# Performance work log

Hardware: AMD Instinct MI355X
Metric: run time of the kernel (lower is better)

## Reference

```python
import jax, jax.numpy as jnp
import numpy as np

EMBED = 768
HEADS = 12
D_K = EMBED // HEADS  # 64


def setup_inputs() -> dict:
    key = jax.random.key(0)
    ks = jax.random.split(key, 9)
    w_scale = EMBED ** -0.5
    inp = {
        "x": jax.random.normal(ks[0], (128, 256, 1, EMBED), dtype=jnp.float32),
        "Wq": jax.random.normal(ks[1], (EMBED, EMBED), dtype=jnp.float32) * w_scale,
        "bq": jax.random.normal(ks[2], (EMBED,), dtype=jnp.float32) * 0.02,
        "Wk": jax.random.normal(ks[3], (EMBED, EMBED), dtype=jnp.float32) * w_scale,
        "bk": jax.random.normal(ks[4], (EMBED,), dtype=jnp.float32) * 0.02,
        "Wv": jax.random.normal(ks[5], (EMBED, EMBED), dtype=jnp.float32) * w_scale,
        "bv": jax.random.normal(ks[6], (EMBED,), dtype=jnp.float32) * 0.02,
        "Wo": jax.random.normal(ks[7], (EMBED, EMBED), dtype=jnp.float32) * w_scale,
        "bo": jax.random.normal(ks[8], (EMBED,), dtype=jnp.float32) * 0.02,
    }
    return inp


def reference(x, Wq, bq, Wk, bk, Wv, bv, Wo, bo):
    # x: (n_rows r, n_cols i/j, batch n, embed)
    R, C, B, E = x.shape
    H, Dk = HEADS, D_K
    # tied-row scaling: d_k^{-1/2} / sqrt(n_rows)
    scaling = (Dk ** -0.5) / np.sqrt(R).astype(np.float32)

    q = (x @ Wq.T + bq).reshape(R, C, B, H, Dk) * scaling
    k = (x @ Wk.T + bk).reshape(R, C, B, H, Dk)
    v = (x @ Wv.T + bv).reshape(R, C, B, H, Dk)

    # scores summed over rows r and head dim d -> (h, n, i, j)
    scores = jnp.einsum('rinhd,rjnhd->hnij', q, k)
    probs = jax.nn.softmax(scores, axis=-1)  # dropout p=0 -> identity

    # shared attention applied per row
    c = jnp.einsum('hnij,rjnhd->rinhd', probs, v).reshape(R, C, B, E)
    out = c @ Wo.T + bo
    return (out, probs)
```

## Files before the change

kernel.cpp:

```cpp
#include <hip/hip_runtime.h>
#include <math.h>

typedef short bf16x8 __attribute__((ext_vector_type(8)));
typedef float f32x4 __attribute__((ext_vector_type(4)));
typedef unsigned short ushort8 __attribute__((ext_vector_type(8)));

constexpr int R = 128, Cc = 256, E = 768, H = 12;
constexpr int M = R * Cc;
constexpr size_t TOK = (size_t)M * E;

__device__ __forceinline__ unsigned short f2b(float f) {
  unsigned int u = __float_as_uint(f);
  u += 0x7fff + ((u >> 16) & 1);
  return (unsigned short)(u >> 16);
}

__device__ __forceinline__ void ldst16(const unsigned short* g, unsigned short* l) {
  __builtin_amdgcn_global_load_lds(
      (const __attribute__((address_space(1))) unsigned int*)g,
      (__attribute__((address_space(3))) unsigned int*)l, 16, 0, 0);
}

__global__ __launch_bounds__(256) void cvt_bf16(const float* __restrict__ in,
                                                unsigned short* __restrict__ out,
                                                int n8) {
  int i = blockIdx.x * 256 + threadIdx.x;
  if (i >= n8) return;
  const float4* p = (const float4*)in;
  float4 a = p[2 * i], b = p[2 * i + 1];
  ushort8 o;
  o[0] = f2b(a.x); o[1] = f2b(a.y); o[2] = f2b(a.z); o[3] = f2b(a.w);
  o[4] = f2b(b.x); o[5] = f2b(b.y); o[6] = f2b(b.z); o[7] = f2b(b.w);
  ((ushort8*)out)[i] = o;
}

template <int MODE>
__global__ __launch_bounds__(256) void proj_mfma(
    const unsigned short* __restrict__ A, const unsigned short* __restrict__ B,
    const float* __restrict__ bias, void* __restrict__ Yv, float scale) {
  constexpr int K = 768, N = 768;
  __shared__ unsigned short As[128 * 32];
  __shared__ unsigned short Bs[128 * 32];
  const int tid = threadIdx.x, wv = tid >> 6, ln = tid & 63;
  const int n0 = blockIdx.x * 128, m0 = blockIdx.y * 128;
  const int wm = (wv & 1) * 64, wn = (wv >> 1) * 64;
  const int srow = ln >> 2, scol = (ln & 3) * 8;
  f32x4 acc[4][4] = {};
  for (int k0 = 0; k0 < K; k0 += 32) {
    __syncthreads();
#pragma unroll
    for (int t = 0; t < 2; ++t) {
      const int ch = wv * 2 + t;
      const int row = ch * 16 + srow;
      ldst16(A + (size_t)(m0 + row) * K + k0 + scol, As + ch * 512 + ln * 8);
      ldst16(B + (size_t)(n0 + row) * K + k0 + scol, Bs + ch * 512 + ln * 8);
    }
    __syncthreads();
    bf16x8 a[4], b[4];
#pragma unroll
    for (int i = 0; i < 4; ++i)
      a[i] = *(const bf16x8*)(As + (wm + i * 16 + (ln & 15)) * 32 + (ln >> 4) * 8);
#pragma unroll
    for (int j = 0; j < 4; ++j)
      b[j] = *(const bf16x8*)(Bs + (wn + j * 16 + (ln & 15)) * 32 + (ln >> 4) * 8);
#pragma unroll
    for (int i = 0; i < 4; ++i)
#pragma unroll
      for (int j = 0; j < 4; ++j)
        acc[i][j] = __builtin_amdgcn_mfma_f32_16x16x32_bf16(a[i], b[j], acc[i][j], 0, 0, 0);
  }
#pragma unroll
  for (int j = 0; j < 4; ++j) {
    const int n = n0 + wn + j * 16 + (ln & 15);
    const float bn = bias[n];
#pragma unroll
    for (int i = 0; i < 4; ++i) {
#pragma unroll
      for (int r = 0; r < 4; ++r) {
        const int m = m0 + wm + i * 16 + (ln >> 4) * 4 + r;
        const float v = (acc[i][j][r] + bn) * scale;
        if (MODE == 0)      ((unsigned short*)Yv)[(size_t)m * N + n] = f2b(v);
        else if (MODE == 1) ((unsigned short*)Yv)[(size_t)n * M + m] = f2b(v);
        else                ((float*)Yv)[(size_t)m * N + n] = v;
      }
    }
  }
}

__global__ __launch_bounds__(256) void qk_mfma(const unsigned short* __restrict__ q,
                                               const unsigned short* __restrict__ k,
                                               float* __restrict__ Sp) {
  __shared__ unsigned short As[64 * 64];
  __shared__ unsigned short Bs[64 * 64];
  const int tid = threadIdx.x, wv = tid >> 6, ln = tid & 63;
  const int i0 = (blockIdx.x & 3) * 64, j0 = (blockIdx.x >> 2) * 64;
  const int h = blockIdx.y, kc = blockIdx.z;
  const int wm = (wv & 1) * 32, wn = (wv >> 1) * 32;
  const int srow = ln >> 3, scol = (ln & 7) * 8;
  f32x4 acc[2][2] = {};
  for (int rr = 0; rr < 32; ++rr) {
    const int r = kc * 32 + rr;
    __syncthreads();
#pragma unroll
    for (int t = 0; t < 2; ++t) {
      const int ch = wv * 2 + t;
      const int row = ch * 8 + srow;
      ldst16(q + (size_t)(r * Cc + i0 + row) * E + h * 64 + scol, As + ch * 512 + ln * 8);
      ldst16(k + (size_t)(r * Cc + j0 + row) * E + h * 64 + scol, Bs + ch * 512 + ln * 8);
    }
    __syncthreads();
#pragma unroll
    for (int dk = 0; dk < 2; ++dk) {
      bf16x8 a[2], b[2];
#pragma unroll
      for (int i = 0; i < 2; ++i)
        a[i] = *(const bf16x8*)(As + (wm + i * 16 + (ln & 15)) * 64 + dk * 32 + (ln >> 4) * 8);
#pragma unroll
      for (int j = 0; j < 2; ++j)
        b[j] = *(const bf16x8*)(Bs + (wn + j * 16 + (ln & 15)) * 64 + dk * 32 + (ln >> 4) * 8);
#pragma unroll
      for (int i = 0; i < 2; ++i)
#pragma unroll
        for (int j = 0; j < 2; ++j)
          acc[i][j] = __builtin_amdgcn_mfma_f32_16x16x32_bf16(a[i], b[j], acc[i][j], 0, 0, 0);
    }
  }
  const size_t base = ((size_t)kc * H + h) * Cc * Cc;
#pragma unroll
  for (int i = 0; i < 2; ++i)
#pragma unroll
    for (int j = 0; j < 2; ++j)
#pragma unroll
      for (int r4 = 0; r4 < 4; ++r4) {
        const int ii = i0 + wm + i * 16 + (ln >> 4) * 4 + r4;
        const int jj = j0 + wn + j * 16 + (ln & 15);
        Sp[base + (size_t)ii * Cc + jj] = acc[i][j][r4];
      }
}

__global__ __launch_bounds__(256) void softmax_k(const float* __restrict__ Sp,
                                                 float* __restrict__ P,
                                                 unsigned short* __restrict__ Pb) {
  const int row = blockIdx.x, j = threadIdx.x;
  const size_t stride = (size_t)H * Cc * Cc;
  const size_t base = (size_t)row * Cc + j;
  float s = Sp[base] + Sp[base + stride] + Sp[base + 2 * stride] + Sp[base + 3 * stride];
  float m = s;
#pragma unroll
  for (int o = 32; o > 0; o >>= 1) m = fmaxf(m, __shfl_xor(m, o));
  __shared__ float sm[4], ss[4];
  const int wid = j >> 6, lane = j & 63;
  if (lane == 0) sm[wid] = m;
  __syncthreads();
  m = fmaxf(fmaxf(sm[0], sm[1]), fmaxf(sm[2], sm[3]));
  float e = expf(s - m);
  float t = e;
#pragma unroll
  for (int o = 32; o > 0; o >>= 1) t += __shfl_xor(t, o);
  if (lane == 0) ss[wid] = t;
  __syncthreads();
  t = ss[0] + ss[1] + ss[2] + ss[3];
  const float p = e / t;
  P[base] = p;
  Pb[base] = f2b(p);
}

__global__ __launch_bounds__(256) void pv_mfma(const unsigned short* __restrict__ P,
                                               const unsigned short* __restrict__ V,
                                               unsigned short* __restrict__ Co) {
  __shared__ unsigned short As[64 * 64];
  __shared__ unsigned short Bs[64 * 64];
  const int tid = threadIdx.x, wv = tid >> 6, ln = tid & 63;
  const int i0 = blockIdx.x * 64;
  const int r = blockIdx.y, h = blockIdx.z;
  const int wm = (wv & 1) * 32, wn = (wv >> 1) * 32;
  const int srow = ln >> 3, scol = (ln & 7) * 8;
  f32x4 acc[2][2] = {};
  for (int jc = 0; jc < 4; ++jc) {
    const int j0 = jc * 64;
    __syncthreads();
#pragma unroll
    for (int t = 0; t < 2; ++t) {
      const int ch = wv * 2 + t;
      const int row = ch * 8 + srow;
      ldst16(P + ((size_t)h * Cc + i0 + row) * Cc + j0 + scol, As + ch * 512 + ln * 8);
      ldst16(V + (size_t)(h * 64 + row) * M + r * Cc + j0 + scol, Bs + ch * 512 + ln * 8);
    }
    __syncthreads();
#pragma unroll
    for (int dk = 0; dk < 2; ++dk) {
      bf16x8 a[2], b[2];
#pragma unroll
      for (int i = 0; i < 2; ++i)
        a[i] = *(const bf16x8*)(As + (wm + i * 16 + (ln & 15)) * 64 + dk * 32 + (ln >> 4) * 8);
#pragma unroll
      for (int j = 0; j < 2; ++j)
        b[j] = *(const bf16x8*)(Bs + (wn + j * 16 + (ln & 15)) * 64 + dk * 32 + (ln >> 4) * 8);
#pragma unroll
      for (int i = 0; i < 2; ++i)
#pragma unroll
        for (int j = 0; j < 2; ++j)
          acc[i][j] = __builtin_amdgcn_mfma_f32_16x16x32_bf16(a[i], b[j], acc[i][j], 0, 0, 0);
    }
  }
#pragma unroll
  for (int i = 0; i < 2; ++i)
#pragma unroll
    for (int j = 0; j < 2; ++j)
#pragma unroll
      for (int r4 = 0; r4 < 4; ++r4) {
        const int mm = i0 + wm + i * 16 + (ln >> 4) * 4 + r4;
        const int nn = wn + j * 16 + (ln & 15);
        Co[((size_t)r * Cc + mm) * E + h * 64 + nn] = f2b(acc[i][j][r4]);
      }
}

extern "C" void kernel_launch(void* const* d_in, const int* in_sizes, int n_in,
                              void* d_out, int out_size, void* d_ws, size_t ws_size,
                              hipStream_t stream) {
  const float* x  = (const float*)d_in[0];
  const float* Wq = (const float*)d_in[1];
  const float* bq = (const float*)d_in[2];
  const float* Wk = (const float*)d_in[3];
  const float* bk = (const float*)d_in[4];
  const float* Wv = (const float*)d_in[5];
  const float* bv = (const float*)d_in[6];
  const float* Wo = (const float*)d_in[7];
  const float* bo = (const float*)d_in[8];
  float* out = (float*)d_out;
  float* probs = out + TOK;

  char* ws = (char*)d_ws;
  unsigned short* x_bf  = (unsigned short*)(ws);
  unsigned short* q_bf  = (unsigned short*)(ws + 50331648);
  unsigned short* k_bf  = (unsigned short*)(ws + 100663296);
  unsigned short* vT_bf = (unsigned short*)(ws + 150994944);
  unsigned short* Wq_bf = (unsigned short*)(ws + 201326592);
  unsigned short* Wk_bf = Wq_bf + 589824;
  unsigned short* Wv_bf = Wk_bf + 589824;
  unsigned short* Wo_bf = Wv_bf + 589824;
  float* S_part         = (float*)(ws + 206045184);
  unsigned short* P_bf  = (unsigned short*)(ws + 218628096);
  unsigned short* c_bf  = q_bf;

  const float scaling = 0.125f / sqrtf(128.f);

  cvt_bf16<<<12288, 256, 0, stream>>>(x, x_bf, 3145728);
  cvt_bf16<<<288, 256, 0, stream>>>(Wq, Wq_bf, 73728);
  cvt_bf16<<<288, 256, 0, stream>>>(Wk, Wk_bf, 73728);
  cvt_bf16<<<288, 256, 0, stream>>>(Wv, Wv_bf, 73728);
  cvt_bf16<<<288, 256, 0, stream>>>(Wo, Wo_bf, 73728);

  dim3 gp(6, 256);
  proj_mfma<0><<<gp, 256, 0, stream>>>(x_bf, Wq_bf, bq, q_bf, scaling);
  proj_mfma<0><<<gp, 256, 0, stream>>>(x_bf, Wk_bf, bk, k_bf, 1.0f);
  proj_mfma<1><<<gp, 256, 0, stream>>>(x_bf, Wv_bf, bv, vT_bf, 1.0f);

  qk_mfma<<<dim3(16, H, 4), 256, 0, stream>>>(q_bf, k_bf, S_part);
  softmax_k<<<H * Cc, 256, 0, stream>>>(S_part, probs, P_bf);
  pv_mfma<<<dim3(4, R, H), 256, 0, stream>>>(P_bf, vT_bf, c_bf);

  proj_mfma<2><<<gp, 256, 0, stream>>>(c_bf, Wo_bf, bo, out, 1.0f);
}
```

Baseline: 539.8 us.

## Fuse QKV projection and relayout Q/K/V for large-tile attention GEMMs

Merges the three Q/K/V projections into one launch over a concatenated weight matrix. Its epilogue writes Q and K in a head-major layout where the row index and head dim form one contiguous reduction axis, and writes V transposed per head. That lets the QK and PV stages run as plain 128x128-tile GEMMs with 64-wide K steps through a shared gemm_core, replacing the small 64x64 tiles that reloaded one row at a time. QK split-K goes from 4 to 8 partials, so softmax sums eight partial score buffers. The cost is scattered 2-byte stores in the projection epilogue and more partial-score traffic.

```diff
diff --git a/kernel.cpp b/kernel.cpp
--- a/kernel.cpp
+++ b/kernel.cpp
@@ -34,107 +34,104 @@
   ((ushort8*)out)[i] = o;
 }
 
-template <int MODE>
-__global__ __launch_bounds__(256) void proj_mfma(
-    const unsigned short* __restrict__ A, const unsigned short* __restrict__ B,
-    const float* __restrict__ bias, void* __restrict__ Yv, float scale) {
-  constexpr int K = 768, N = 768;
-  __shared__ unsigned short As[128 * 32];
-  __shared__ unsigned short Bs[128 * 32];
-  const int tid = threadIdx.x, wv = tid >> 6, ln = tid & 63;
-  const int n0 = blockIdx.x * 128, m0 = blockIdx.y * 128;
-  const int wm = (wv & 1) * 64, wn = (wv >> 1) * 64;
-  const int srow = ln >> 2, scol = (ln & 3) * 8;
-  f32x4 acc[4][4] = {};
-  for (int k0 = 0; k0 < K; k0 += 32) {
+template <int KITERS>
+__device__ __forceinline__ void gemm_core(
+    const unsigned short* __restrict__ Aptr, size_t Astride,
+    const unsigned short* __restrict__ Bptr, size_t Bstride,
+    unsigned short* As, unsigned short* Bs, int wv, int ln, f32x4 acc[4][4]) {
+  const int srow = ln >> 3, scol = (ln & 7) * 8;
+  const int wm = (wv & 1) * 64, wn = (wv >> 1) * 64;
+#pragma unroll 1
+  for (int kt = 0; kt < KITERS; ++kt) {
+    const int k0 = kt * 64;
     __syncthreads();
 #pragma unroll
-    for (int t = 0; t < 2; ++t) {
-      const int ch = wv * 2 + t;
-      const int row = ch * 16 + srow;
-      ldst16(A + (size_t)(m0 + row) * K + k0 + scol, As + ch * 512 + ln * 8);
-      ldst16(B + (size_t)(n0 + row) * K + k0 + scol, Bs + ch * 512 + ln * 8);
+    for (int t = 0; t < 4; ++t) {
+      const int ch = wv * 4 + t;
+      const int row = ch * 8 + srow;
+      ldst16(Aptr + (size_t)row * Astride + k0 + scol, As + ch * 512 + ln * 8);
+      ldst16(Bptr + (size_t)row * Bstride + k0 + scol, Bs + ch * 512 + ln * 8);
     }
     __syncthreads();
-    bf16x8 a[4], b[4];
-#pragma unroll
-    for (int i = 0; i < 4; ++i)
-      a[i] = *(const bf16x8*)(As + (wm + i * 16 + (ln & 15)) * 32 + (ln >> 4) * 8);
-#pragma unroll
-    for (int j = 0; j < 4; ++j)
-      b[j] = *(const bf16x8*)(Bs + (wn + j * 16 + (ln & 15)) * 32 + (ln >> 4) * 8);
-#pragma unroll
-    for (int i = 0; i < 4; ++i)
+#pragma unroll
+    for (int dk = 0; dk < 2; ++dk) {
+      bf16x8 a[4], b[4];
+#pragma unroll
+      for (int i = 0; i < 4; ++i)
+        a[i] = *(const bf16x8*)(As + (wm + i * 16 + (ln & 15)) * 64 + dk * 32 + (ln >> 4) * 8);
 #pragma unroll
       for (int j = 0; j < 4; ++j)
-        acc[i][j] = __builtin_amdgcn_mfma_f32_16x16x32_bf16(a[i], b[j], acc[i][j], 0, 0, 0);
-  }
+        b[j] = *(const bf16x8*)(Bs + (wn + j * 16 + (ln & 15)) * 64 + dk * 32 + (ln >> 4) * 8);
+#pragma unroll
+      for (int i = 0; i < 4; ++i)
+#pragma unroll
+        for (int j = 0; j < 4; ++j)
+          acc[i][j] = __builtin_amdgcn_mfma_f32_16x16x32_bf16(a[i], b[j], acc[i][j], 0, 0, 0);
+    }
+  }
+}
+
+__global__ __launch_bounds__(256) void qkv_mfma(
+    const unsigned short* __restrict__ A, const unsigned short* __restrict__ B,
+    const float* __restrict__ bq, const float* __restrict__ bk,
+    const float* __restrict__ bv, unsigned short* __restrict__ qp,
+    unsigned short* __restrict__ kp, unsigned short* __restrict__ vp, float scale) {
+  __shared__ unsigned short As[128 * 64];
+  __shared__ unsigned short Bs[128 * 64];
+  const int tid = threadIdx.x, wv = tid >> 6, ln = tid & 63;
+  const int n0 = blockIdx.x * 128, m0 = blockIdx.y * 128;
+  const int wm = (wv & 1) * 64, wn = (wv >> 1) * 64;
+  f32x4 acc[4][4] = {};
+  gemm_core<12>(A + (size_t)m0 * E, E, B + (size_t)n0 * E, E, As, Bs, wv, ln, acc);
+  const int part = n0 / 768;
+  const float* bias = part == 0 ? bq : (part == 1 ? bk : bv);
+  const float sc = part == 0 ? scale : 1.0f;
 #pragma unroll
   for (int j = 0; j < 4; ++j) {
     const int n = n0 + wn + j * 16 + (ln & 15);
-    const float bn = bias[n];
-#pragma unroll
-    for (int i = 0; i < 4; ++i) {
-#pragma unroll
-      for (int r = 0; r < 4; ++r) {
-        const int m = m0 + wm + i * 16 + (ln >> 4) * 4 + r;
-        const float v = (acc[i][j][r] + bn) * scale;
-        if (MODE == 0)      ((unsigned short*)Yv)[(size_t)m * N + n] = f2b(v);
-        else if (MODE == 1) ((unsigned short*)Yv)[(size_t)n * M + m] = f2b(v);
-        else                ((float*)Yv)[(size_t)m * N + n] = v;
-      }
-    }
-  }
-}
-
-__global__ __launch_bounds__(256) void qk_mfma(const unsigned short* __restrict__ q,
-                                               const unsigned short* __restrict__ k,
+    const int nn = n - part * 768;
+    const int h = nn >> 6, d = nn & 63;
+    const float bn = bias[nn];
+#pragma unroll
+    for (int i = 0; i < 4; ++i)
+#pragma unroll
+      for (int r4 = 0; r4 < 4; ++r4) {
+        const int m = m0 + wm + i * 16 + (ln >> 4) * 4 + r4;
+        const int r = m >> 8, ii = m & 255;
+        const unsigned short val = f2b((acc[i][j][r4] + bn) * sc);
+        if (part == 0)
+          qp[((size_t)(h * 256 + ii) << 13) + r * 64 + d] = val;
+        else if (part == 1)
+          kp[((size_t)(h * 256 + ii) << 13) + r * 64 + d] = val;
+        else
+          vp[((size_t)(h * 8192 + r * 64 + d) << 8) + ii] = val;
+      }
+  }
+}
+
+__global__ __launch_bounds__(256) void qk_mfma(const unsigned short* __restrict__ qp,
+                                               const unsigned short* __restrict__ kp,
                                                float* __restrict__ Sp) {
-  __shared__ unsigned short As[64 * 64];
-  __shared__ unsigned short Bs[64 * 64];
-  const int tid = threadIdx.x, wv = tid >> 6, ln = tid & 63;
-  const int i0 = (blockIdx.x & 3) * 64, j0 = (blockIdx.x >> 2) * 64;
+  __shared__ unsigned short As[128 * 64];
+  __shared__ unsigned short Bs[128 * 64];
+  const int tid = threadIdx.x, wv = tid >> 6, ln = tid & 63;
+  const int m0 = (blockIdx.x & 1) * 128, n0 = (blockIdx.x >> 1) * 128;
   const int h = blockIdx.y, kc = blockIdx.z;
-  const int wm = (wv & 1) * 32, wn = (wv >> 1) * 32;
-  const int srow = ln >> 3, scol = (ln & 7) * 8;
-  f32x4 acc[2][2] = {};
-  for (int rr = 0; rr < 32; ++rr) {
-    const int r = kc * 32 + rr;
-    __syncthreads();
-#pragma unroll
-    for (int t = 0; t < 2; ++t) {
-      const int ch = wv * 2 + t;
-      const int row = ch * 8 + srow;
-      ldst16(q + (size_t)(r * Cc + i0 + row) * E + h * 64 + scol, As + ch * 512 + ln * 8);
-      ldst16(k + (size_t)(r * Cc + j0 + row) * E + h * 64 + scol, Bs + ch * 512 + ln * 8);
-    }
-    __syncthreads();
-#pragma unroll
-    for (int dk = 0; dk < 2; ++dk) {
-      bf16x8 a[2], b[2];
-#pragma unroll
-      for (int i = 0; i < 2; ++i)
-        a[i] = *(const bf16x8*)(As + (wm + i * 16 + (ln & 15)) * 64 + dk * 32 + (ln >> 4) * 8);
-#pragma unroll
-      for (int j = 0; j < 2; ++j)
-        b[j] = *(const bf16x8*)(Bs + (wn + j * 16 + (ln & 15)) * 64 + dk * 32 + (ln >> 4) * 8);
-#pragma unroll
-      for (int i = 0; i < 2; ++i)
-#pragma unroll
-        for (int j = 0; j < 2; ++j)
-          acc[i][j] = __builtin_amdgcn_mfma_f32_16x16x32_bf16(a[i], b[j], acc[i][j], 0, 0, 0);
-    }
-  }
-  const size_t base = ((size_t)kc * H + h) * Cc * Cc;
-#pragma unroll
-  for (int i = 0; i < 2; ++i)
-#pragma unroll
-    for (int j = 0; j < 2; ++j)
-#pragma unroll
-      for (int r4 = 0; r4 < 4; ++r4) {
-        const int ii = i0 + wm + i * 16 + (ln >> 4) * 4 + r4;
-        const int jj = j0 + wn + j * 16 + (ln & 15);
-        Sp[base + (size_t)ii * Cc + jj] = acc[i][j][r4];
+  const int wm = (wv & 1) * 64, wn = (wv >> 1) * 64;
+  f32x4 acc[4][4] = {};
+  const size_t hb = (size_t)h * 256 * 8192 + kc * 1024;
+  gemm_core<16>(qp + hb + (size_t)m0 * 8192, 8192,
+                kp + hb + (size_t)n0 * 8192, 8192, As, Bs, wv, ln, acc);
+  float* out = Sp + ((size_t)kc * H + h) * Cc * Cc;
+#pragma unroll
+  for (int i = 0; i < 4; ++i)
+#pragma unroll
+    for (int j = 0; j < 4; ++j)
+#pragma unroll
+      for (int r4 = 0; r4 < 4; ++r4) {
+        const int mm = m0 + wm + i * 16 + (ln >> 4) * 4 + r4;
+        const int nn = n0 + wn + j * 16 + (ln & 15);
+        out[(size_t)mm * Cc + nn] = acc[i][j][r4];
       }
 }
 
@@ -144,7 +141,9 @@
   const int row = blockIdx.x, j = threadIdx.x;
   const size_t stride = (size_t)H * Cc * Cc;
   const size_t base = (size_t)row * Cc + j;
-  float s = Sp[base] + Sp[base + stride] + Sp[base + 2 * stride] + Sp[base + 3 * stride];
+  float s = 0.f;
+#pragma unroll
+  for (int kc = 0; kc < 8; ++kc) s += Sp[base + kc * stride];
   float m = s;
 #pragma unroll
   for (int o = 32; o > 0; o >>= 1) m = fmaxf(m, __shfl_xor(m, o));
@@ -168,51 +167,52 @@
 __global__ __launch_bounds__(256) void pv_mfma(const unsigned short* __restrict__ P,
                                                const unsigned short* __restrict__ V,
                                                unsigned short* __restrict__ Co) {
-  __shared__ unsigned short As[64 * 64];
-  __shared__ unsigned short Bs[64 * 64];
-  const int tid = threadIdx.x, wv = tid >> 6, ln = tid & 63;
-  const int i0 = blockIdx.x * 64;
-  const int r = blockIdx.y, h = blockIdx.z;
-  const int wm = (wv & 1) * 32, wn = (wv >> 1) * 32;
-  const int srow = ln >> 3, scol = (ln & 7) * 8;
-  f32x4 acc[2][2] = {};
-  for (int jc = 0; jc < 4; ++jc) {
-    const int j0 = jc * 64;
-    __syncthreads();
-#pragma unroll
-    for (int t = 0; t < 2; ++t) {
-      const int ch = wv * 2 + t;
-      const int row = ch * 8 + srow;
-      ldst16(P + ((size_t)h * Cc + i0 + row) * Cc + j0 + scol, As + ch * 512 + ln * 8);
-      ldst16(V + (size_t)(h * 64 + row) * M + r * Cc + j0 + scol, Bs + ch * 512 + ln * 8);
-    }
-    __syncthreads();
-#pragma unroll
-    for (int dk = 0; dk < 2; ++dk) {
-      bf16x8 a[2], b[2];
-#pragma unroll
-      for (int i = 0; i < 2; ++i)
-        a[i] = *(const bf16x8*)(As + (wm + i * 16 + (ln & 15)) * 64 + dk * 32 + (ln >> 4) * 8);
-#pragma unroll
-      for (int j = 0; j < 2; ++j)
-        b[j] = *(const bf16x8*)(Bs + (wn + j * 16 + (ln & 15)) * 64 + dk * 32 + (ln >> 4) * 8);
-#pragma unroll
-      for (int i = 0; i < 2; ++i)
-#pragma unroll
-        for (int j = 0; j < 2; ++j)
-          acc[i][j] = __builtin_amdgcn_mfma_f32_16x16x32_bf16(a[i], b[j], acc[i][j], 0, 0, 0);
-    }
-  }
-#pragma unroll
-  for (int i = 0; i < 2; ++i)
-#pragma unroll
-    for (int j = 0; j < 2; ++j)
-#pragma unroll
-      for (int r4 = 0; r4 < 4; ++r4) {
-        const int mm = i0 + wm + i * 16 + (ln >> 4) * 4 + r4;
-        const int nn = wn + j * 16 + (ln & 15);
-        Co[((size_t)r * Cc + mm) * E + h * 64 + nn] = f2b(acc[i][j][r4]);
-      }
+  __shared__ unsigned short As[128 * 64];
+  __shared__ unsigned short Bs[128 * 64];
+  const int tid = threadIdx.x, wv = tid >> 6, ln = tid & 63;
+  const int m0 = (blockIdx.x & 1) * 128, n0 = (blockIdx.x >> 1) * 128;
+  const int h = blockIdx.y;
+  const int wm = (wv & 1) * 64, wn = (wv >> 1) * 64;
+  f32x4 acc[4][4] = {};
+  gemm_core<4>(P + (size_t)h * 65536 + (size_t)m0 * 256, 256,
+               V + ((size_t)h * 8192 + n0) * 256, 256, As, Bs, wv, ln, acc);
+#pragma unroll
+  for (int j = 0; j < 4; ++j) {
+    const int n = n0 + wn + j * 16 + (ln & 15);
+    const int r = n >> 6, d = n & 63;
+#pragma unroll
+    for (int i = 0; i < 4; ++i)
+#pragma unroll
+      for (int r4 = 0; r4 < 4; ++r4) {
+        const int ii = m0 + wm + i * 16 + (ln >> 4) * 4 + r4;
+        Co[((size_t)(r * 256 + ii)) * E + h * 64 + d] = f2b(acc[i][j][r4]);
+      }
+  }
+}
+
+__global__ __launch_bounds__(256) void out_mfma(const unsigned short* __restrict__ A,
+                                                const unsigned short* __restrict__ B,
+                                                const float* __restrict__ bias,
+                                                float* __restrict__ Y) {
+  __shared__ unsigned short As[128 * 64];
+  __shared__ unsigned short Bs[128 * 64];
+  const int tid = threadIdx.x, wv = tid >> 6, ln = tid & 63;
+  const int n0 = blockIdx.x * 128, m0 = blockIdx.y * 128;
+  const int wm = (wv & 1) * 64, wn = (wv >> 1) * 64;
+  f32x4 acc[4][4] = {};
+  gemm_core<12>(A + (size_t)m0 * E, E, B + (size_t)n0 * E, E, As, Bs, wv, ln, acc);
+#pragma unroll
+  for (int j = 0; j < 4; ++j) {
+    const int n = n0 + wn + j * 16 + (ln & 15);
+    const float bn = bias[n];
+#pragma unroll
+    for (int i = 0; i < 4; ++i)
+#pragma unroll
+      for (int r4 = 0; r4 < 4; ++r4) {
+        const int m = m0 + wm + i * 16 + (ln >> 4) * 4 + r4;
+        Y[(size_t)m * E + n] = acc[i][j][r4] + bn;
+      }
+  }
 }
 
 extern "C" void kernel_launch(void* const* d_in, const int* in_sizes, int n_in,
@@ -231,34 +231,27 @@
   float* probs = out + TOK;
 
   char* ws = (char*)d_ws;
-  unsigned short* x_bf  = (unsigned short*)(ws);
-  unsigned short* q_bf  = (unsigned short*)(ws + 50331648);
-  unsigned short* k_bf  = (unsigned short*)(ws + 100663296);
-  unsigned short* vT_bf = (unsigned short*)(ws + 150994944);
-  unsigned short* Wq_bf = (unsigned short*)(ws + 201326592);
-  unsigned short* Wk_bf = Wq_bf + 589824;
-  unsigned short* Wv_bf = Wk_bf + 589824;
-  unsigned short* Wo_bf = Wv_bf + 589824;
-  float* S_part         = (float*)(ws + 206045184);
-  unsigned short* P_bf  = (unsigned short*)(ws + 218628096);
-  unsigned short* c_bf  = q_bf;
+  unsigned short* x_bf   = (unsigned short*)(ws);
+  unsigned short* qp     = (unsigned short*)(ws + 50331648);
+  unsigned short* kp     = (unsigned short*)(ws + 100663296);
+  unsigned short* vp     = (unsigned short*)(ws + 150994944);
+  unsigned short* Wqkv   = (unsigned short*)(ws + 201326592);
+  unsigned short* Wo_bf  = (unsigned short*)(ws + 204865536);
+  float* S_part          = (float*)(ws + 206045184);
+  unsigned short* P_bf   = (unsigned short*)(ws + 231211008);
+  unsigned short* c_bf   = (unsigned short*)(ws + 232783872);
 
   const float scaling = 0.125f / sqrtf(128.f);
 
   cvt_bf16<<<12288, 256, 0, stream>>>(x, x_bf, 3145728);
-  cvt_bf16<<<288, 256, 0, stream>>>(Wq, Wq_bf, 73728);
-  cvt_bf16<<<288, 256, 0, stream>>>(Wk, Wk_bf, 73728);
-  cvt_bf16<<<288, 256, 0, stream>>>(Wv, Wv_bf, 73728);
+  cvt_bf16<<<288, 256, 0, stream>>>(Wq, Wqkv, 73728);
+  cvt_bf16<<<288, 256, 0, stream>>>(Wk, Wqkv + 589824, 73728);
+  cvt_bf16<<<288, 256, 0, stream>>>(Wv, Wqkv + 1179648, 73728);
   cvt_bf16<<<288, 256, 0, stream>>>(Wo, Wo_bf, 73728);
 
-  dim3 gp(6, 256);
-  proj_mfma<0><<<gp, 256, 0, stream>>>(x_bf, Wq_bf, bq, q_bf, scaling);
-  proj_mfma<0><<<gp, 256, 0, stream>>>(x_bf, Wk_bf, bk, k_bf, 1.0f);
-  proj_mfma<1><<<gp, 256, 0, stream>>>(x_bf, Wv_bf, bv, vT_bf, 1.0f);
-
-  qk_mfma<<<dim3(16, H, 4), 256, 0, stream>>>(q_bf, k_bf, S_part);
+  qkv_mfma<<<dim3(18, 256), 256, 0, stream>>>(x_bf, Wqkv, bq, bk, bv, qp, kp, vp, scaling);
+  qk_mfma<<<dim3(4, H, 8), 256, 0, stream>>>(qp, kp, S_part);
   softmax_k<<<H * Cc, 256, 0, stream>>>(S_part, probs, P_bf);
-  pv_mfma<<<dim3(4, R, H), 256, 0, stream>>>(P_bf, vT_bf, c_bf);
-
-  proj_mfma<2><<<gp, 256, 0, stream>>>(c_bf, Wo_bf, bo, out, 1.0f);
-}
+  pv_mfma<<<dim3(128, H), 256, 0, stream>>>(P_bf, vp, c_bf);
+  out_mfma<<<dim3(6, 256), 256, 0, stream>>>(c_bf, Wo_bf, bo, out);
+}
```

New measurement: 583.8 us. +8.2%, slower.
